# Kernel tuning notes

Hardware: AMD Instinct MI355X
Metric: run time of the kernel (lower is better)

The kernel has to match this reference:

```python
import jax, jax.numpy as jnp
import numpy as np

D_MODEL = 2048
N_HEADS = 16
D_HEAD = 128
B = 2
S = 2048


def setup_inputs() -> dict:
    key = jax.random.key(0)
    ks = jax.random.split(key, 9)
    sc_in = 1.0 / np.sqrt(D_MODEL)
    sc_hd = 1.0 / np.sqrt(N_HEADS * D_HEAD)
    return {
        "x": jax.random.normal(ks[0], (B, S, D_MODEL), dtype=jnp.float32),
        "Wq": jax.random.normal(ks[1], (D_MODEL, N_HEADS * D_HEAD), dtype=jnp.float32) * sc_in,
        "bq": jax.random.normal(ks[2], (N_HEADS * D_HEAD,), dtype=jnp.float32) * 0.01,
        "Wk": jax.random.normal(ks[3], (D_MODEL, N_HEADS * D_HEAD), dtype=jnp.float32) * sc_in,
        "bk": jax.random.normal(ks[4], (N_HEADS * D_HEAD,), dtype=jnp.float32) * 0.01,
        "Wv": jax.random.normal(ks[5], (D_MODEL, N_HEADS * D_HEAD), dtype=jnp.float32) * sc_in,
        "bv": jax.random.normal(ks[6], (N_HEADS * D_HEAD,), dtype=jnp.float32) * 0.01,
        "Wo": jax.random.normal(ks[7], (N_HEADS * D_HEAD, D_MODEL), dtype=jnp.float32) * sc_hd,
        "bo": jax.random.normal(ks[8], (D_MODEL,), dtype=jnp.float32) * 0.01,
    }


def reference(x, Wq, bq, Wk, bk, Wv, bv, Wo, bo):
    b, s, _ = x.shape
    # projections -> [b, s, h, d] -> [b, h, s, d]
    q = (x @ Wq + bq).reshape(b, s, N_HEADS, D_HEAD).transpose(0, 2, 1, 3)
    k = (x @ Wk + bk).reshape(b, s, N_HEADS, D_HEAD).transpose(0, 2, 1, 3)
    v = (x @ Wv + bv).reshape(b, s, N_HEADS, D_HEAD).transpose(0, 2, 1, 3)
    scale = 1.0 / jnp.sqrt(jnp.asarray(D_HEAD, dtype=x.dtype))
    scores = jnp.einsum("bhsd,bhtd->bhst", q, k) * scale  # [b,h,s,s]
    causal = jnp.triu(jnp.ones((s, s), dtype=bool), k=1)
    scores = jnp.where(causal, jnp.asarray(-jnp.inf, dtype=scores.dtype), scores)
    attn = jax.nn.softmax(scores, axis=-1)
    ctx = jnp.einsum("bhst,bhtd->bhsd", attn, v)  # [b,h,s,d]
    ctx = ctx.transpose(0, 2, 1, 3).reshape(b, s, N_HEADS * D_HEAD)
    return ctx @ Wo + bo
```

## Files before the change

### kernel.cpp

```cpp
#include <hip/hip_runtime.h>
#include <hip/hip_bf16.h>
#include <stdint.h>

#define S_LEN  2048
#define DMODEL 2048
#define NHEADS 16
#define DHEAD  128
#define NBATCH 2
#define MROWS  (NBATCH * S_LEN)

typedef __bf16 bf16_t;
typedef __bf16 bf16x8 __attribute__((ext_vector_type(8)));
typedef float  f32x4  __attribute__((ext_vector_type(4)));
typedef float  f32x16 __attribute__((ext_vector_type(16)));

#define MFMA_BF16(A, B, C) __builtin_amdgcn_mfma_f32_16x16x32_bf16((A), (B), (C), 0, 0, 0)
#define MFMA32(A, B, C)    __builtin_amdgcn_mfma_f32_32x32x16_bf16((A), (B), (C), 0, 0, 0)

__device__ __forceinline__ void gload_lds16(const void* g, void* l) {
  __builtin_amdgcn_global_load_lds(
      (__attribute__((address_space(1))) uint32_t*)(uintptr_t)g,
      (__attribute__((address_space(3))) uint32_t*)l,
      16, 0, 0);
}

__device__ __forceinline__ unsigned pk2(float lo, float hi) {
  const unsigned short a = __builtin_bit_cast(unsigned short, (bf16_t)lo);
  const unsigned short b = __builtin_bit_cast(unsigned short, (bf16_t)hi);
  return (unsigned)a | ((unsigned)b << 16);
}

__global__ __launch_bounds__(256) void cast_kernel(const float* __restrict__ X,
                                                   bf16_t* __restrict__ Xb) {
  const int i = blockIdx.x * 256 + threadIdx.x;
  const f32x4 a = ((const f32x4*)X)[2 * i];
  const f32x4 b = ((const f32x4*)X)[2 * i + 1];
  bf16x8 o;
#pragma unroll
  for (int j = 0; j < 4; ++j) { o[j] = (bf16_t)a[j]; o[j + 4] = (bf16_t)b[j]; }
  ((bf16x8*)Xb)[i] = o;
}

__global__ __launch_bounds__(256) void transpose_cast(
    const float* __restrict__ W0, const float* __restrict__ W1,
    const float* __restrict__ W2, const float* __restrict__ W3,
    bf16_t* __restrict__ T0, bf16_t* __restrict__ T1,
    bf16_t* __restrict__ T2, bf16_t* __restrict__ T3) {
  const float* W; bf16_t* T;
  switch (blockIdx.z) {
    case 0:  W = W0; T = T0; break;
    case 1:  W = W1; T = T1; break;
    case 2:  W = W2; T = T2; break;
    default: W = W3; T = T3; break;
  }
  __shared__ float tile[64][65];
  const int r0 = blockIdx.y * 64;
  const int c0 = blockIdx.x * 64;
  const int tx = threadIdx.x & 63;
  const int ty = threadIdx.x >> 6;
#pragma unroll
  for (int i = 0; i < 16; ++i) {
    const int r = ty + i * 4;
    tile[r][tx] = W[(size_t)(r0 + r) * DMODEL + c0 + tx];
  }
  __syncthreads();
#pragma unroll
  for (int i = 0; i < 16; ++i) {
    const int r = ty + i * 4;
    T[(size_t)(c0 + r) * DMODEL + r0 + tx] = (bf16_t)tile[tx][r];
  }
}

__global__ __launch_bounds__(256) void transpose_v(const bf16_t* __restrict__ V,
                                                   bf16_t* __restrict__ VT) {
  __shared__ bf16_t tile[64 * 64];
  const int bh = blockIdx.z;
  const int s0 = blockIdx.x * 64;
  const int d0 = blockIdx.y * 64;
  const bf16_t* src = V + ((size_t)bh * S_LEN + s0) * DHEAD + d0;
#pragma unroll
  for (int i = 0; i < 2; ++i) {
    const int v = threadIdx.x + i * 256;
    const int r = v >> 3, ch = v & 7;
    *(bf16x8*)&tile[r * 64 + ((ch ^ ((r >> 3) & 7)) << 3)] =
        *(const bf16x8*)(src + (size_t)r * DHEAD + ch * 8);
  }
  __syncthreads();
  bf16_t* dst = VT + ((size_t)bh * DHEAD + d0) * S_LEN + s0;
#pragma unroll
  for (int i = 0; i < 2; ++i) {
    const int v = threadIdx.x + i * 256;
    const int d = v >> 3, j = v & 7;
    bf16x8 o;
#pragma unroll
    for (int e = 0; e < 8; ++e) {
      const int row = j * 8 + e;
      o[e] = tile[row * 64 + (((d >> 3) ^ j) << 3) + (d & 7)];
    }
    *(bf16x8*)(dst + (size_t)d * S_LEN + j * 8) = o;
  }
}

template <int MODE>
__device__ __forceinline__ void gemm8_body(const bf16_t* __restrict__ A,
                                           const bf16_t* __restrict__ Bt,
                                           const float* __restrict__ bias,
                                           void* __restrict__ out) {
  __shared__ __align__(16) char lds8[2 * 49152];
  const int tid  = threadIdx.x;
  const int lane = tid & 63;
  const int w    = tid >> 6;
  const int g    = lane >> 4;
  const int l16  = lane & 15;
  const int wm   = w >> 2;
  const int wn   = w & 3;
  const int m0   = blockIdx.y * 128;
  const int n0   = blockIdx.x * 256;

  f32x4 acc[4][4];
#pragma unroll
  for (int i = 0; i < 4; ++i)
#pragma unroll
    for (int j = 0; j < 4; ++j) acc[i][j] = (f32x4){0.f, 0.f, 0.f, 0.f};

  const int st_r0 = tid >> 3;
  const int st_ch = tid & 7;

  auto stage = [&](int tile, int r) {
    if (tile >= DMODEL / 64) return;
    const int kt = tile << 6;
    char* db = lds8 + (tile & 1) * 49152 + r * 16384 + w * 1024;
    const bf16_t* sb = (r == 0) ? (A + (size_t)m0 * DMODEL + kt)
                                : (Bt + (size_t)(n0 + ((r - 1) << 7)) * DMODEL + kt);
#pragma unroll
    for (int jj = 0; jj < 2; ++jj) {
      const int row = jj * 64 + st_r0;
      gload_lds16(sb + (size_t)row * DMODEL + ((st_ch ^ (row & 7)) << 3),
                  db + jj * 8192);
    }
  };

  stage(0, 0); stage(0, 1); stage(0, 2); stage(1, 0);
  asm volatile("s_waitcnt vmcnt(2)" ::: "memory");
  __builtin_amdgcn_s_barrier();

#pragma unroll 2
  for (int t = 0; t < DMODEL / 64; ++t) {
    const char* cb = lds8 + (t & 1) * 49152;
    bf16x8 af[4][2], b0[2][2], b1[2][2];
#pragma unroll
    for (int i = 0; i < 4; ++i) {
      const int row = wm * 64 + i * 16 + l16;
      const char* rp = cb + row * 128;
#pragma unroll
      for (int ks = 0; ks < 2; ++ks)
        af[i][ks] = *(const bf16x8*)(rp + ((((ks << 2) | g) ^ (row & 7)) << 4));
    }
#pragma unroll
    for (int j = 0; j < 2; ++j) {
      const int row = (wn & 1) * 64 + j * 16 + l16;
      const char* rp = cb + 16384 + (wn >> 1) * 16384 + row * 128;
#pragma unroll
      for (int ks = 0; ks < 2; ++ks)
        b0[j][ks] = *(const bf16x8*)(rp + ((((ks << 2) | g) ^ (row & 7)) << 4));
    }
    stage(t + 1, 1); stage(t + 1, 2);
    __builtin_amdgcn_s_barrier();
    asm volatile("s_waitcnt lgkmcnt(0)" ::: "memory");
    __builtin_amdgcn_s_setprio(1);
#pragma unroll
    for (int i = 0; i < 4; ++i)
#pragma unroll
      for (int j = 0; j < 2; ++j) {
        acc[i][j] = MFMA_BF16(af[i][0], b0[j][0], acc[i][j]);
        acc[i][j] = MFMA_BF16(af[i][1], b0[j][1], acc[i][j]);
      }
    __builtin_amdgcn_s_setprio(0);
    __builtin_amdgcn_s_barrier();
#pragma unroll
    for (int j = 0; j < 2; ++j) {
      const int row = (wn & 1) * 64 + (j + 2) * 16 + l16;
      const char* rp = cb + 16384 + (wn >> 1) * 16384 + row * 128;
#pragma unroll
      for (int ks = 0; ks < 2; ++ks)
        b1[j][ks] = *(const bf16x8*)(rp + ((((ks << 2) | g) ^ (row & 7)) << 4));
    }
    stage(t + 2, 0);
    __builtin_amdgcn_s_barrier();
    asm volatile("s_waitcnt lgkmcnt(0)" ::: "memory");
    __builtin_amdgcn_s_setprio(1);
#pragma unroll
    for (int i = 0; i < 4; ++i)
#pragma unroll
      for (int j = 0; j < 2; ++j) {
        acc[i][j + 2] = MFMA_BF16(af[i][0], b1[j][0], acc[i][j + 2]);
        acc[i][j + 2] = MFMA_BF16(af[i][1], b1[j][1], acc[i][j + 2]);
      }
    __builtin_amdgcn_s_setprio(0);
    if (t < DMODEL / 64 - 2) asm volatile("s_waitcnt vmcnt(2)" ::: "memory");
    else                     asm volatile("s_waitcnt vmcnt(0)" ::: "memory");
    __builtin_amdgcn_s_barrier();
  }

#pragma unroll
  for (int i = 0; i < 4; ++i) {
#pragma unroll
    for (int j = 0; j < 4; ++j) {
      const int n    = n0 + wn * 64 + j * 16 + l16;
      const float bb = bias[n];
#pragma unroll
      for (int r = 0; r < 4; ++r) {
        const int m   = m0 + wm * 64 + i * 16 + g * 4 + r;
        const float v = acc[i][j][r] + bb;
        if (MODE == 0) {
          const int b = m >> 11, s = m & (S_LEN - 1);
          const int h = n >> 7,  d = n & (DHEAD - 1);
          ((bf16_t*)out)[((size_t)(b * NHEADS + h) * S_LEN + s) * DHEAD + d] = (bf16_t)v;
        } else {
          ((float*)out)[(size_t)m * DMODEL + n] = v;
        }
      }
    }
  }
}

__global__ __launch_bounds__(512, 2) void gemm_qkv(
    const bf16_t* __restrict__ Xb,
    const bf16_t* __restrict__ WqT, const bf16_t* __restrict__ WkT,
    const bf16_t* __restrict__ WvT,
    const float* __restrict__ bq, const float* __restrict__ bk,
    const float* __restrict__ bv,
    bf16_t* __restrict__ Qg, bf16_t* __restrict__ Kg, bf16_t* __restrict__ Vg) {
  const bf16_t* Bt; const float* bias; bf16_t* out;
  if (blockIdx.z == 0)      { Bt = WqT; bias = bq; out = Qg; }
  else if (blockIdx.z == 1) { Bt = WkT; bias = bk; out = Kg; }
  else                      { Bt = WvT; bias = bv; out = Vg; }
  gemm8_body<0>(Xb, Bt, bias, out);
}

__global__ __launch_bounds__(512, 2) void gemm_out(
    const bf16_t* __restrict__ Ctx, const bf16_t* __restrict__ WoT,
    const float* __restrict__ bo, float* __restrict__ out) {
  gemm8_body<1>(Ctx, WoT, bo, out);
}

#define KLDS_BYTES (64 * 272)
#define VLDS_BYTES (128 * 144)
#define BUF_BYTES  (KLDS_BYTES + VLDS_BYTES)

__global__ __launch_bounds__(256, 2) void attn_kernel(
    const bf16_t* __restrict__ Qg, const bf16_t* __restrict__ Kg,
    const bf16_t* __restrict__ VTg, bf16_t* __restrict__ ctx) {
  __shared__ __align__(16) char ldsbuf[2][BUF_BYTES];
  __shared__ float lbuf[4][32];

  const int tid  = threadIdx.x;
  const int lane = tid & 63;
  const int w    = tid >> 6;
  const int l31  = lane & 31;
  const int hi   = lane >> 5;

  const int id   = blockIdx.x;
  const int bh   = id & 31;
  const int jraw = id >> 5;
  const int j    = (jraw < 8) ? jraw : 23 - jraw;
  const int q0   = j * 128;
  const int qw   = q0 + w * 32;
  const int tq   = (qw + 31) >> 6;
  const int NT   = (q0 + 128) >> 6;

  const size_t bho = (size_t)bh * S_LEN * DHEAD;
  const bf16_t* Qb  = Qg + bho;
  const bf16_t* Kb  = Kg + bho;
  const bf16_t* VTb = VTg + bho;

  bf16x8 qreg[8];
#pragma unroll
  for (int s = 0; s < 8; ++s)
    qreg[s] = *(const bf16x8*)(Qb + (size_t)(qw + l31) * DHEAD + s * 16 + hi * 8);

  f32x16 oacc[4];
#pragma unroll
  for (int d0 = 0; d0 < 4; ++d0)
#pragma unroll
    for (int e = 0; e < 16; ++e) oacc[d0][e] = 0.f;

  float m = -1e30f, lsum = 0.f;
  const float sc2 = 0.12751751135f;

  bf16x8 kst[4], vst[4];
#pragma unroll
  for (int i = 0; i < 4; ++i) {
    const int c = tid + i * 256;
    kst[i] = *(const bf16x8*)(Kb + (size_t)(c >> 4) * DHEAD + (c & 15) * 8);
    vst[i] = *(const bf16x8*)(VTb + (size_t)(c >> 3) * S_LEN + (c & 7) * 8);
  }
#pragma unroll
  for (int i = 0; i < 4; ++i) {
    const int c  = tid + i * 256;
    const int kr = c >> 4, kc = c & 15;
    *(bf16x8*)(ldsbuf[0] + kr * 272 + ((kc ^ ((kr >> 3) & 3)) << 4)) = kst[i];
    const int vr = c >> 3, vc = c & 7;
    *(bf16x8*)(ldsbuf[0] + KLDS_BYTES + vr * 144 + ((vc ^ ((vr >> 3) & 3)) << 4)) = vst[i];
  }
  __syncthreads();

  for (int t = 0; t < NT; ++t) {
    const int kt = t << 6;
    const char* bK = ldsbuf[t & 1];
    const char* bV = bK + KLDS_BYTES;
    const bool hn = (t + 1 < NT);
    if (hn) {
#pragma unroll
      for (int i = 0; i < 4; ++i) {
        const int c = tid + i * 256;
        kst[i] = *(const bf16x8*)(Kb + (size_t)(kt + 64 + (c >> 4)) * DHEAD + (c & 15) * 8);
        vst[i] = *(const bf16x8*)(VTb + (size_t)(c >> 3) * S_LEN + kt + 64 + (c & 7) * 8);
      }
    }

    if (t <= tq) {
      f32x16 stt[2];
#pragma unroll
      for (int kh = 0; kh < 2; ++kh)
#pragma unroll
        for (int e = 0; e < 16; ++e) stt[kh][e] = 0.f;
#pragma unroll
      for (int kh = 0; kh < 2; ++kh) {
        const int row = kh * 32 + l31;
        const char* rb = bK + row * 272;
        const int swz = ((row >> 3) & 3) << 4;
#pragma unroll
        for (int s = 0; s < 8; ++s) {
          const bf16x8 kf = *(const bf16x8*)(rb + ((((s << 1) | hi) << 4) ^ swz));
          stt[kh] = MFMA32(kf, qreg[s], stt[kh]);
        }
      }
      if (t == tq) {
        const int qg = qw + l31;
#pragma unroll
        for (int kh = 0; kh < 2; ++kh)
#pragma unroll
          for (int r = 0; r < 16; ++r) {
            const int kv = kt + kh * 32 + (r & 3) + 8 * (r >> 2) + 4 * hi;
            stt[kh][r] = (kv > qg) ? -1e30f : stt[kh][r];
          }
      }
      float pm = stt[0][0];
#pragma unroll
      for (int kh = 0; kh < 2; ++kh)
#pragma unroll
        for (int r = 0; r < 16; ++r)
          if (kh | r) pm = fmaxf(pm, stt[kh][r]);
      pm = fmaxf(pm, __shfl_xor(pm, 32));
      const float pmax = pm * sc2;
      if (!__all(pmax <= m + 8.f)) {
        const float mn   = fmaxf(m, pmax);
        const float corr = __builtin_amdgcn_exp2f(m - mn);
        m = mn;
        lsum *= corr;
        if (!hi) lbuf[w][l31] = corr;
#pragma unroll
        for (int r = 0; r < 16; ++r) {
          const float cr = lbuf[w][(r & 3) + 8 * (r >> 2) + 4 * hi];
#pragma unroll
          for (int d0 = 0; d0 < 4; ++d0) oacc[d0][r] *= cr;
        }
      }
      float rs = 0.f;
#pragma unroll
      for (int kh = 0; kh < 2; ++kh)
#pragma unroll
        for (int r = 0; r < 16; ++r) {
          const float p = __builtin_amdgcn_exp2f(__builtin_fmaf(stt[kh][r], sc2, -m));
          stt[kh][r] = p;
          rs += p;
        }
      rs += __shfl_xor(rs, 32);
      lsum += rs;
      unsigned pw_[2][8];
#pragma unroll
      for (int kh = 0; kh < 2; ++kh)
#pragma unroll
        for (int jj = 0; jj < 8; ++jj)
          pw_[kh][jj] = pk2(stt[kh][2 * jj], stt[kh][2 * jj + 1]);
      bf16x8 pa[4];
#pragma unroll
      for (int kh = 0; kh < 2; ++kh)
#pragma unroll
        for (int c2 = 0; c2 < 2; ++c2) {
          const unsigned o0 = pw_[kh][4 * c2 + 0], o1 = pw_[kh][4 * c2 + 1];
          const unsigned o2 = pw_[kh][4 * c2 + 2], o3 = pw_[kh][4 * c2 + 3];
          const unsigned p0 = (unsigned)__shfl_xor((int)o0, 32);
          const unsigned p1 = (unsigned)__shfl_xor((int)o1, 32);
          const unsigned p2 = (unsigned)__shfl_xor((int)o2, 32);
          const unsigned p3 = (unsigned)__shfl_xor((int)o3, 32);
          union { unsigned u[4]; bf16x8 v; } uu;
          uu.u[0] = hi ? p2 : o0;
          uu.u[1] = hi ? p3 : o1;
          uu.u[2] = hi ? o2 : p0;
          uu.u[3] = hi ? o3 : p1;
          pa[2 * kh + c2] = uu.v;
        }
#pragma unroll
      for (int d0 = 0; d0 < 4; ++d0) {
        const int row = d0 * 32 + l31;
        const char* rb = bV + row * 144;
        const int swz = ((row >> 3) & 3) << 4;
#pragma unroll
        for (int ks = 0; ks < 4; ++ks) {
          const bf16x8 vb = *(const bf16x8*)(rb + ((((ks << 1) | hi) << 4) ^ swz));
          oacc[d0] = MFMA32(pa[ks], vb, oacc[d0]);
        }
      }
    }
    __syncthreads();
    if (hn) {
      char* nB = ldsbuf[(t + 1) & 1];
#pragma unroll
      for (int i = 0; i < 4; ++i) {
        const int c  = tid + i * 256;
        const int kr = c >> 4, kc = c & 15;
        *(bf16x8*)(nB + kr * 272 + ((kc ^ ((kr >> 3) & 3)) << 4)) = kst[i];
        const int vr = c >> 3, vc = c & 7;
        *(bf16x8*)(nB + KLDS_BYTES + vr * 144 + ((vc ^ ((vr >> 3) & 3)) << 4)) = vst[i];
      }
    }
    __syncthreads();
  }

  if (!hi) lbuf[w][l31] = 1.0f / lsum;
  const int b = bh >> 4, h = bh & 15;
#pragma unroll
  for (int r = 0; r < 16; ++r) {
    const int cro = (r & 3) + 8 * (r >> 2) + 4 * hi;
    const float li = lbuf[w][cro];
    const size_t base = ((size_t)(b * S_LEN + qw + cro)) * DMODEL + h * DHEAD;
#pragma unroll
    for (int d0 = 0; d0 < 4; ++d0)
      ctx[base + d0 * 32 + l31] = (bf16_t)(oacc[d0][r] * li);
  }
}

extern "C" void kernel_launch(void* const* d_in, const int* in_sizes, int n_in,
                              void* d_out, int out_size, void* d_ws, size_t ws_size,
                              hipStream_t stream) {
  const float* x  = (const float*)d_in[0];
  const float* Wq = (const float*)d_in[1];
  const float* bq = (const float*)d_in[2];
  const float* Wk = (const float*)d_in[3];
  const float* bk = (const float*)d_in[4];
  const float* Wv = (const float*)d_in[5];
  const float* bv = (const float*)d_in[6];
  const float* Wo = (const float*)d_in[7];
  const float* bo = (const float*)d_in[8];

  char* ws = (char*)d_ws;
  const size_t MB = 1ull << 20;
  bf16_t* Xb  = (bf16_t*)(ws + 0);
  bf16_t* VTg = (bf16_t*)(ws + 0);
  bf16_t* WqT = (bf16_t*)(ws + 16 * MB);
  bf16_t* WkT = (bf16_t*)(ws + 24 * MB);
  bf16_t* WvT = (bf16_t*)(ws + 32 * MB);
  bf16_t* WoT = (bf16_t*)(ws + 40 * MB);
  bf16_t* Qg  = (bf16_t*)(ws + 48 * MB);
  bf16_t* Kg  = (bf16_t*)(ws + 64 * MB);
  bf16_t* Vg  = (bf16_t*)(ws + 80 * MB);
  bf16_t* Ctx = (bf16_t*)(ws + 96 * MB);
  if (ws_size < 112 * MB) return;

  cast_kernel<<<dim3(MROWS * DMODEL / (256 * 8)), 256, 0, stream>>>(x, Xb);
  transpose_cast<<<dim3(32, 32, 4), 256, 0, stream>>>(Wq, Wk, Wv, Wo, WqT, WkT, WvT, WoT);
  gemm_qkv<<<dim3(DMODEL / 256, MROWS / 128, 3), 512, 0, stream>>>(
      Xb, WqT, WkT, WvT, bq, bk, bv, Qg, Kg, Vg);
  transpose_v<<<dim3(32, 2, 32), 256, 0, stream>>>(Vg, VTg);
  attn_kernel<<<dim3(512), 256, 0, stream>>>(Qg, Kg, VTg, Ctx);
  gemm_out<<<dim3(DMODEL / 256, MROWS / 128), 512, 0, stream>>>(Ctx, WoT, bo, (float*)d_out);
}
```

Before: 235.1 us.

## Rewrite QKV GEMM with 256x256 tiles, phased LDS pipeline and XCD-aware block mapping

```diff
diff --git a/kernel.cpp b/kernel.cpp
--- a/kernel.cpp
+++ b/kernel.cpp
@@ -98,6 +98,120 @@
       o[e] = tile[row * 64 + (((d >> 3) ^ j) << 3) + (d & 7)];
     }
     *(bf16x8*)(dst + (size_t)d * S_LEN + j * 8) = o;
+  }
+}
+
+#define VMCNT(N) asm volatile("s_waitcnt vmcnt(" #N ")" ::: "memory")
+
+#define QPHASE(T, P, N) do {                                                     \
+  VMCNT(N);                                                                      \
+  __builtin_amdgcn_s_barrier();                                                  \
+  asm volatile("" ::: "memory");                                                 \
+  {                                                                              \
+    const char* regA = lds + ((T) & 1) * 65536 + ((P) >> 1) * 32768;             \
+    const char* regB = regA + 16384;                                             \
+    if (((P) & 1) == 0) {                                                        \
+      _Pragma("unroll")                                                          \
+      for (int j = 0; j < 4; ++j)                                                \
+        bf[j] = *(const bf16x8*)(regB + (wn * 64 + j * 16 + l16) * 64 + g * 16); \
+    }                                                                            \
+    bf16x8 af[4];                                                                \
+    _Pragma("unroll")                                                            \
+    for (int i = 0; i < 4; ++i)                                                  \
+      af[i] = *(const bf16x8*)(regA + (wm * 128 + (((P) & 1) * 4 + i) * 16 + l16) * 64 + g * 16); \
+    stage((T) + 1, (P));                                                         \
+    __builtin_amdgcn_s_setprio(1);                                               \
+    _Pragma("unroll")                                                            \
+    for (int i = 0; i < 4; ++i) {                                                \
+      _Pragma("unroll")                                                          \
+      for (int j = 0; j < 4; ++j)                                                \
+        acc[((P) & 1) * 4 + i][j] =                                              \
+            MFMA_BF16(af[i], bf[j], acc[((P) & 1) * 4 + i][j]);                  \
+    }                                                                            \
+    __builtin_amdgcn_s_setprio(0);                                               \
+  }                                                                              \
+} while (0)
+
+__global__ __launch_bounds__(512, 2) void gemm_qkv(
+    const bf16_t* __restrict__ Xb,
+    const bf16_t* __restrict__ WqT, const bf16_t* __restrict__ WkT,
+    const bf16_t* __restrict__ WvT,
+    const float* __restrict__ bq, const float* __restrict__ bk,
+    const float* __restrict__ bv,
+    bf16_t* __restrict__ Qg, bf16_t* __restrict__ Kg, bf16_t* __restrict__ Vg) {
+  __shared__ __align__(16) char lds[2 * 65536];
+
+  const int tid  = threadIdx.x;
+  const int lane = tid & 63;
+  const int w    = tid >> 6;
+  const int g    = lane >> 4;
+  const int l16  = lane & 15;
+  const int wm   = w >> 2;
+  const int wn   = w & 3;
+
+  const int bid = blockIdx.x;
+  const int wg  = (bid & 7) * 48 + (bid >> 3);
+  const int mi  = wg / 24;
+  const int ni  = wg % 24;
+  const int z0  = ni >> 3;
+  const bf16_t* Bt = (z0 == 0) ? WqT : (z0 == 1) ? WkT : WvT;
+  const bf16_t* Abase = Xb + (size_t)mi * 256 * DMODEL;
+  const bf16_t* Bbase = Bt + (size_t)(ni & 7) * 256 * DMODEL;
+
+  f32x4 acc[8][4];
+#pragma unroll
+  for (int i = 0; i < 8; ++i)
+#pragma unroll
+    for (int j = 0; j < 4; ++j) acc[i][j] = (f32x4){0.f, 0.f, 0.f, 0.f};
+
+  auto stage = [&](int tile, int p) {
+    if (tile >= DMODEL / 64) return;
+    const int kh = p >> 1, mat = p & 1;
+    const int kt = tile * 64 + kh * 32;
+    const bf16_t* src = mat ? Bbase : Abase;
+    char* dstbase = lds + (tile & 1) * 65536 + kh * 32768 + mat * 16384;
+#pragma unroll
+    for (int jj = 0; jj < 2; ++jj) {
+      const int c = jj * 512 + tid;
+      gload_lds16(src + (size_t)(c >> 2) * DMODEL + kt + (c & 3) * 8,
+                  dstbase + (jj * 512 + (tid & ~63)) * 16);
+    }
+  };
+
+  stage(0, 0); stage(0, 1); stage(0, 2); stage(0, 3);
+
+  bf16x8 bf[4];
+  for (int t = 0; t < DMODEL / 64 - 1; ++t) {
+    QPHASE(t, 0, 4);
+    QPHASE(t, 1, 6);
+    QPHASE(t, 2, 4);
+    QPHASE(t, 3, 6);
+  }
+  {
+    const int t = DMODEL / 64 - 1;
+    QPHASE(t, 0, 4);
+    QPHASE(t, 1, 4);
+    QPHASE(t, 2, 2);
+    QPHASE(t, 3, 0);
+  }
+
+  const float* bias = (z0 == 0) ? bq : (z0 == 1) ? bk : bv;
+  bf16_t* outb      = (z0 == 0) ? Qg : (z0 == 1) ? Kg : Vg;
+#pragma unroll
+  for (int i = 0; i < 8; ++i) {
+#pragma unroll
+    for (int j = 0; j < 4; ++j) {
+      const int nloc = (ni & 7) * 256 + wn * 64 + j * 16 + l16;
+      const float bb = bias[nloc];
+      const int h = nloc >> 7, d = nloc & (DHEAD - 1);
+#pragma unroll
+      for (int r = 0; r < 4; ++r) {
+        const int mrow = mi * 256 + wm * 128 + i * 16 + g * 4 + r;
+        const int b = mrow >> 11, s = mrow & (S_LEN - 1);
+        outb[((size_t)(b * NHEADS + h) * S_LEN + s) * DHEAD + d] =
+            (bf16_t)(acc[i][j][r] + bb);
+      }
+    }
   }
 }
 
@@ -224,20 +338,6 @@
   }
 }
 
-__global__ __launch_bounds__(512, 2) void gemm_qkv(
-    const bf16_t* __restrict__ Xb,
-    const bf16_t* __restrict__ WqT, const bf16_t* __restrict__ WkT,
-    const bf16_t* __restrict__ WvT,
-    const float* __restrict__ bq, const float* __restrict__ bk,
-    const float* __restrict__ bv,
-    bf16_t* __restrict__ Qg, bf16_t* __restrict__ Kg, bf16_t* __restrict__ Vg) {
-  const bf16_t* Bt; const float* bias; bf16_t* out;
-  if (blockIdx.z == 0)      { Bt = WqT; bias = bq; out = Qg; }
-  else if (blockIdx.z == 1) { Bt = WkT; bias = bk; out = Kg; }
-  else                      { Bt = WvT; bias = bv; out = Vg; }
-  gemm8_body<0>(Xb, Bt, bias, out);
-}
-
 __global__ __launch_bounds__(512, 2) void gemm_out(
     const bf16_t* __restrict__ Ctx, const bf16_t* __restrict__ WoT,
     const float* __restrict__ bo, float* __restrict__ out) {
@@ -471,7 +571,7 @@
 
   cast_kernel<<<dim3(MROWS * DMODEL / (256 * 8)), 256, 0, stream>>>(x, Xb);
   transpose_cast<<<dim3(32, 32, 4), 256, 0, stream>>>(Wq, Wk, Wv, Wo, WqT, WkT, WvT, WoT);
-  gemm_qkv<<<dim3(DMODEL / 256, MROWS / 128, 3), 512, 0, stream>>>(
+  gemm_qkv<<<dim3(384), 512, 0, stream>>>(
       Xb, WqT, WkT, WvT, bq, bk, bv, Qg, Kg, Vg);
   transpose_v<<<dim3(32, 2, 32), 256, 0, stream>>>(Vg, VTg);
   attn_kernel<<<dim3(512), 256, 0, stream>>>(Qg, Kg, VTg, Ctx);
```

Result: slower. 246.4 us (+4.8%).

## Stage attention K/V tiles via direct global-to-LDS async loads

Applied to the files above, without the earlier changes.

```diff
diff --git a/kernel.cpp b/kernel.cpp
--- a/kernel.cpp
+++ b/kernel.cpp
@@ -244,14 +244,14 @@
   gemm8_body<1>(Ctx, WoT, bo, out);
 }
 
-#define KLDS_BYTES (64 * 272)
-#define VLDS_BYTES (128 * 144)
-#define BUF_BYTES  (KLDS_BYTES + VLDS_BYTES)
+#define KTILE_B 16384
+#define VTILE_B 16384
+#define ABUF_B  (KTILE_B + VTILE_B)
 
 __global__ __launch_bounds__(256, 2) void attn_kernel(
     const bf16_t* __restrict__ Qg, const bf16_t* __restrict__ Kg,
     const bf16_t* __restrict__ VTg, bf16_t* __restrict__ ctx) {
-  __shared__ __align__(16) char ldsbuf[2][BUF_BYTES];
+  __shared__ __align__(16) char ldsbuf[2][ABUF_B];
   __shared__ float lbuf[4][32];
 
   const int tid  = threadIdx.x;
@@ -274,6 +274,25 @@
   const bf16_t* Kb  = Kg + bho;
   const bf16_t* VTb = VTg + bho;
 
+  auto stageT = [&](int t) {
+    const int kt = t << 6;
+    char* dst = ldsbuf[t & 1];
+#pragma unroll
+    for (int i = 0; i < 4; ++i) {
+      const int c   = i * 256 + tid;
+      const int row = c >> 4, ch = c & 15;
+      gload_lds16(Kb + (size_t)(kt + row) * DHEAD + ((ch ^ (row & 7)) << 3),
+                  dst + (i * 256 + (tid & ~63)) * 16);
+    }
+#pragma unroll
+    for (int i = 0; i < 4; ++i) {
+      const int c   = i * 256 + tid;
+      const int row = c >> 3, ch = c & 7;
+      gload_lds16(VTb + (size_t)row * S_LEN + kt + ((ch ^ (row & 7)) << 3),
+                  dst + KTILE_B + (i * 256 + (tid & ~63)) * 16);
+    }
+  };
+
   bf16x8 qreg[8];
 #pragma unroll
   for (int s = 0; s < 8; ++s)
@@ -288,38 +307,17 @@
   float m = -1e30f, lsum = 0.f;
   const float sc2 = 0.12751751135f;
 
-  bf16x8 kst[4], vst[4];
-#pragma unroll
-  for (int i = 0; i < 4; ++i) {
-    const int c = tid + i * 256;
-    kst[i] = *(const bf16x8*)(Kb + (size_t)(c >> 4) * DHEAD + (c & 15) * 8);
-    vst[i] = *(const bf16x8*)(VTb + (size_t)(c >> 3) * S_LEN + (c & 7) * 8);
-  }
-#pragma unroll
-  for (int i = 0; i < 4; ++i) {
-    const int c  = tid + i * 256;
-    const int kr = c >> 4, kc = c & 15;
-    *(bf16x8*)(ldsbuf[0] + kr * 272 + ((kc ^ ((kr >> 3) & 3)) << 4)) = kst[i];
-    const int vr = c >> 3, vc = c & 7;
-    *(bf16x8*)(ldsbuf[0] + KLDS_BYTES + vr * 144 + ((vc ^ ((vr >> 3) & 3)) << 4)) = vst[i];
-  }
+  stageT(0);
+  asm volatile("s_waitcnt vmcnt(0)" ::: "memory");
   __syncthreads();
 
   for (int t = 0; t < NT; ++t) {
-    const int kt = t << 6;
     const char* bK = ldsbuf[t & 1];
-    const char* bV = bK + KLDS_BYTES;
-    const bool hn = (t + 1 < NT);
-    if (hn) {
-#pragma unroll
-      for (int i = 0; i < 4; ++i) {
-        const int c = tid + i * 256;
-        kst[i] = *(const bf16x8*)(Kb + (size_t)(kt + 64 + (c >> 4)) * DHEAD + (c & 15) * 8);
-        vst[i] = *(const bf16x8*)(VTb + (size_t)(c >> 3) * S_LEN + kt + 64 + (c & 7) * 8);
-      }
-    }
+    const char* bV = bK + KTILE_B;
+    if (t + 1 < NT) stageT(t + 1);
 
     if (t <= tq) {
+      const int kt = t << 6;
       f32x16 stt[2];
 #pragma unroll
       for (int kh = 0; kh < 2; ++kh)
@@ -328,8 +326,8 @@
 #pragma unroll
       for (int kh = 0; kh < 2; ++kh) {
         const int row = kh * 32 + l31;
-        const char* rb = bK + row * 272;
-        const int swz = ((row >> 3) & 3) << 4;
+        const char* rb = bK + row * 256;
+        const int swz = (row & 7) << 4;
 #pragma unroll
         for (int s = 0; s < 8; ++s) {
           const bf16x8 kf = *(const bf16x8*)(rb + ((((s << 1) | hi) << 4) ^ swz));
@@ -405,8 +403,8 @@
 #pragma unroll
       for (int d0 = 0; d0 < 4; ++d0) {
         const int row = d0 * 32 + l31;
-        const char* rb = bV + row * 144;
-        const int swz = ((row >> 3) & 3) << 4;
+        const char* rb = bV + row * 128;
+        const int swz = (row & 7) << 4;
 #pragma unroll
         for (int ks = 0; ks < 4; ++ks) {
           const bf16x8 vb = *(const bf16x8*)(rb + ((((ks << 1) | hi) << 4) ^ swz));
@@ -414,18 +412,7 @@
         }
       }
     }
-    __syncthreads();
-    if (hn) {
-      char* nB = ldsbuf[(t + 1) & 1];
-#pragma unroll
-      for (int i = 0; i < 4; ++i) {
-        const int c  = tid + i * 256;
-        const int kr = c >> 4, kc = c & 15;
-        *(bf16x8*)(nB + kr * 272 + ((kc ^ ((kr >> 3) & 3)) << 4)) = kst[i];
-        const int vr = c >> 3, vc = c & 7;
-        *(bf16x8*)(nB + KLDS_BYTES + vr * 144 + ((vc ^ ((vr >> 3) & 3)) << 4)) = vst[i];
-      }
-    }
+    asm volatile("s_waitcnt vmcnt(0)" ::: "memory");
     __syncthreads();
   }
 
```

Measured after the change: 231.4 us. No clear change (-1.6%).
